# Optimization experiments

Measured on AMD Instinct MI355X. Metric: run time of the kernel, lower is better.

## Reference

```python
import jax, jax.numpy as jnp
import numpy as np

EPS = 1e-5

def layernorm(x):
    mu = jnp.mean(x, axis=-1, keepdims=True)
    var = jnp.var(x, axis=-1, keepdims=True)
    return (x - mu) * jax.lax.rsqrt(var + EPS)

def jagged_to_padded(values, offsets, n):
    # values: [T, D]; offsets: [B+1]; -> [B, n, D] zero-padded
    lengths = offsets[1:] - offsets[:-1]            # [B]
    pos = jnp.arange(n)                             # [n]
    idx = offsets[:-1, None] + pos[None, :]         # [B, n]
    mask = pos[None, :] < lengths[:, None]          # [B, n]
    idx = jnp.clip(idx, 0, values.shape[0] - 1)
    return values[idx] * mask[..., None].astype(values.dtype)

def dense_to_jagged(padded, offsets, total):
    t = jnp.arange(total)
    b = jnp.searchsorted(offsets, t, side='right') - 1   # row of each token
    p = t - offsets[b]                                   # position within row
    return padded[b, p]

def causal_conv(x, w, b):
    # x: [B, n, D]; w: [D, D, 3]; residual + bias + leaky_relu
    xt = jnp.transpose(x, (0, 2, 1))                     # [B, D, n]
    xt = jnp.pad(xt, ((0, 0), (0, 0), (2, 0)))           # causal left pad (k-1)
    y = jax.lax.conv_general_dilated(xt, w, (1,), 'VALID',
                                     dimension_numbers=('NCH', 'OIH', 'NCH'))
    y = y + b[None, :, None]
    y = jnp.transpose(y, (0, 2, 1)) + x                  # residual
    return jax.nn.leaky_relu(y, 0.01)

def setup_inputs() -> dict:
    key = jax.random.key(0)
    ks = jax.random.split(key, 8)
    B, n, D = 32, 4096, 256
    P, H, dA = 512, 8, 64
    T = B * (n // 2)  # equal lengths of 2048
    offsets = (jnp.arange(B + 1, dtype=jnp.int64 if jax.config.read('jax_enable_x64') else jnp.int32) * (n // 2)).astype(jnp.int32)
    return {
        'normed_x': jax.random.normal(ks[0], (T, D), dtype=jnp.float32),
        'conv_w': 0.02 * jax.random.normal(ks[1], (D, D, 3), dtype=jnp.float32),
        'conv_b': 0.02 * jax.random.normal(ks[2], (D,), dtype=jnp.float32),
        'pattern': 0.02 * jax.random.normal(ks[3], (P, D), dtype=jnp.float32),
        'wq': 0.02 * jax.random.normal(ks[4], (H * dA, D), dtype=jnp.float32),
        'wkv': 0.02 * jax.random.normal(ks[5], (2 * H * dA, D), dtype=jnp.float32),
        'wout': jax.random.uniform(ks[6], (D, H * dA), dtype=jnp.float32,
                                   minval=-1.0, maxval=1.0) * np.sqrt(6.0 / (D + H * dA)),
        'bout': jnp.zeros((D,), dtype=jnp.float32),
        'x_offsets': offsets,
        'n': n,
    }

def reference(normed_x, conv_w, conv_b, pattern, wq, wkv, wout, bout, x_offsets, n):
    H, dA = 8, 64
    scale = dA ** (-0.5)
    T = normed_x.shape[0]
    # jagged -> padded, causal conv (residual + leaky_relu), padded -> jagged
    padded = jagged_to_padded(normed_x, x_offsets, n)        # [B, n, D]
    padded = causal_conv(padded, conv_w, conv_b)
    x = dense_to_jagged(padded, x_offsets, T)                # [T, D]
    # pattern layernormed twice (SPRM.forward then xattn.forward)
    pat = layernorm(layernorm(pattern))                      # [P, D]
    x = layernorm(x)
    q = (x @ wq.T).reshape(T, H, dA)                         # [T, H, dA]
    kv = (pat @ wkv.T).reshape(pat.shape[0], H, 2 * dA)
    k, v = kv[..., :dA], kv[..., dA:]                        # [P, H, dA]
    scores = scale * jnp.einsum('nhd,whd->nhw', q, k)        # [T, H, P]
    attn = jax.nn.softmax(scores, axis=-1)
    out = jnp.einsum('nhw,whd->nhd', attn, v).reshape(T, H * dA)
    out = out @ wout.T + bout                                # [T, D]
    return layernorm(out)
```

## Files before the change

kernel.cpp:

```cpp
#include <hip/hip_runtime.h>
#include <hip/hip_bf16.h>
#include <math.h>


#define EPSF 1e-5f

typedef short  s16x8 __attribute__((ext_vector_type(8)));
typedef short  s16x4 __attribute__((ext_vector_type(4)));
typedef float  f32x4 __attribute__((ext_vector_type(4)));

typedef __attribute__((address_space(3))) unsigned int       lds_u32_t;
typedef __attribute__((address_space(1))) const unsigned int glb_u32_t;

__device__ __forceinline__ void gload_lds16(const void* g, void* l) {
    __builtin_amdgcn_global_load_lds((glb_u32_t*)g, (lds_u32_t*)l, 16, 0, 0);
}

__device__ __forceinline__ unsigned short f2bf(float f) {
    union { float f; unsigned u; } v; v.f = f;
    unsigned r = (v.u + 0x7fffu + ((v.u >> 16) & 1u)) >> 16;
    return (unsigned short)r;
}
__device__ __forceinline__ float bf2f(unsigned short h) {
    union { unsigned u; float f; } v; v.u = ((unsigned)h) << 16;
    return v.f;
}
__device__ __forceinline__ unsigned fbits(float f) {
    union { float f; unsigned u; } v; v.f = f; return v.u;
}
__device__ __forceinline__ unsigned pk_hi(float lo, float hi) {
    return __builtin_amdgcn_perm(fbits(hi), fbits(lo), 0x07060302u);
}
__device__ __forceinline__ int inv32(int t) {
    return (t & ~31) | ((t & 0x0C) << 1) | ((t & 0x10) >> 2) | (t & 3);
}

union Bfrag { unsigned u[4]; s16x8 s; };

__global__ void cvt_kernel(const float* __restrict__ wq,
                           const float* __restrict__ wout,
                           const float* __restrict__ cw,
                           short* __restrict__ wq_bf,
                           short* __restrict__ wout_bf,
                           short* __restrict__ wck) {
    const int b = blockIdx.x, tid = threadIdx.x;
    if (b < 256) {
        const int i = ((b & 127) * 256 + tid) * 4;
        const float* src = (b < 128) ? wq : wout;
        short* dst = (b < 128) ? wq_bf : wout_bf;
        const float4 x = *(const float4*)(src + i);
        s16x4 o; o[0] = f2bf(x.x); o[1] = f2bf(x.y); o[2] = f2bf(x.z); o[3] = f2bf(x.w);
        *(s16x4*)(dst + i) = o;
    } else {
        const int idx = (b - 256) * 256 + tid;
        const float* p = cw + (size_t)idx * 3;
        wck[idx]              = (short)f2bf(p[0]);
        wck[65536 + idx]      = (short)f2bf(p[1]);
        wck[131072 + idx]     = (short)f2bf(p[2]);
    }
}

__global__ void pat_kv_kernel(const float* __restrict__ pattern,
                              const float* __restrict__ wkv,
                              short* __restrict__ k_bf,
                              short* __restrict__ v_t) {
    __shared__ __align__(16) float spat[256];
    __shared__ float scr[4];
    const int w = blockIdx.x;
    const int tid = threadIdx.x;
    const int lane = tid & 63, wav = tid >> 6;

    float v = pattern[(size_t)w * 256 + tid];

    float s = v;
    #pragma unroll
    for (int off = 32; off; off >>= 1) s += __shfl_xor(s, off);
    if (lane == 0) scr[wav] = s;
    __syncthreads();
    float mu = (scr[0] + scr[1] + scr[2] + scr[3]) * (1.f / 256.f);
    __syncthreads();
    float d = v - mu;
    float s2 = d * d;
    #pragma unroll
    for (int off = 32; off; off >>= 1) s2 += __shfl_xor(s2, off);
    if (lane == 0) scr[wav] = s2;
    __syncthreads();
    float var = (scr[0] + scr[1] + scr[2] + scr[3]) * (1.f / 256.f);
    float x1 = d * rsqrtf(var + EPSF);
    __syncthreads();

    s = x1;
    #pragma unroll
    for (int off = 32; off; off >>= 1) s += __shfl_xor(s, off);
    if (lane == 0) scr[wav] = s;
    __syncthreads();
    mu = (scr[0] + scr[1] + scr[2] + scr[3]) * (1.f / 256.f);
    __syncthreads();
    d = x1 - mu;
    s2 = d * d;
    #pragma unroll
    for (int off = 32; off; off >>= 1) s2 += __shfl_xor(s2, off);
    if (lane == 0) scr[wav] = s2;
    __syncthreads();
    var = (scr[0] + scr[1] + scr[2] + scr[3]) * (1.f / 256.f);
    float x2 = d * rsqrtf(var + EPSF);

    spat[tid] = x2;
    __syncthreads();

    #pragma unroll
    for (int u = 0; u < 4; u++) {
        const int j = tid + 256 * u;
        const float* wr = wkv + (size_t)j * 256;
        float acc = 0.f;
        for (int i4 = 0; i4 < 64; i4++) {
            float4 w4 = *(const float4*)(wr + i4 * 4);
            float4 x4 = *(const float4*)(&spat[i4 * 4]);
            acc += w4.x * x4.x + w4.y * x4.y + w4.z * x4.z + w4.w * x4.w;
        }
        const int h = j >> 7, r = j & 127;
        if (r < 64) {
            const int c = inv32(r);
            const int ck = w >> 7, crow = w & 127;
            const int un = c >> 3, ph = un ^ (crow & 7);
            k_bf[(size_t)h * 32768 + ck * 8192 + crow * 64 + ph * 8 + (c & 7)]
                = (short)f2bf(acc * 0.125f);
        } else {
            const int rd = r - 64;
            const int c = inv32(w);
            const int ck = c >> 7, cc = c & 127;
            const int un = cc >> 3, ph = un ^ (rd & 15);
            v_t[(size_t)h * 32768 + ck * 8192 + rd * 128 + ph * 8 + (cc & 7)]
                = (short)f2bf(acc);
        }
    }
}

__global__ __launch_bounds__(256, 4)
void conv_ln_kernel(const float* __restrict__ x,
                    const short* __restrict__ wck,
                    const float* __restrict__ cb,
                    short* __restrict__ xn_bf) {
    __shared__ __align__(16) short xs[66 * 268];
    const int tid = threadIdx.x;
    const int r0 = blockIdx.x * 64;
    const int pos0 = r0 & 2047;

    #pragma unroll
    for (int it = 0; it < 17; it++) {
        const int idx = tid + it * 256;
        if (idx < 4224) {
            const int row = idx >> 6, c4 = idx & 63;
            float4 v = {0.f, 0.f, 0.f, 0.f};
            if (pos0 - 2 + row >= 0)
                v = *(const float4*)(x + (size_t)(r0 - 2 + row) * 256 + c4 * 4);
            s16x4 o; o[0] = f2bf(v.x); o[1] = f2bf(v.y); o[2] = f2bf(v.z); o[3] = f2bf(v.w);
            *(s16x4*)(xs + row * 268 + c4 * 4) = o;
        }
    }
    __syncthreads();

    const int lane = tid & 63, w = tid >> 6, g = lane >> 4, cl = lane & 15;

    f32x4 acc[4][4];
    #pragma unroll
    for (int mt = 0; mt < 4; mt++)
        #pragma unroll
        for (int nt = 0; nt < 4; nt++) acc[mt][nt] = (f32x4){0.f, 0.f, 0.f, 0.f};

    #pragma unroll
    for (int kk = 0; kk < 3; kk++) {
        const short* wb = wck + kk * 65536;
        for (int s = 0; s < 8; s++) {
            s16x8 a[4];
            #pragma unroll
            for (int mt = 0; mt < 4; mt++)
                a[mt] = *(const s16x8*)(xs + (mt * 16 + cl + kk) * 268 + s * 32 + g * 8);
            #pragma unroll
            for (int nt = 0; nt < 4; nt++) {
                const s16x8 b = *(const s16x8*)(wb + (size_t)(w * 64 + nt * 16 + cl) * 256 + s * 32 + g * 8);
                #pragma unroll
                for (int mt = 0; mt < 4; mt++)
                    acc[mt][nt] = __builtin_amdgcn_mfma_f32_16x16x32_bf16(a[mt], b, acc[mt][nt], 0, 0, 0);
            }
        }
    }

    #pragma unroll
    for (int nt = 0; nt < 4; nt++) {
        const int col = w * 64 + nt * 16 + cl;
        const float b = cb[col];
        #pragma unroll
        for (int mt = 0; mt < 4; mt++)
            #pragma unroll
            for (int r = 0; r < 4; r++) {
                const int row = mt * 16 + g * 4 + r;
                float y = acc[mt][nt][r] + b + x[(size_t)(r0 + row) * 256 + col];
                acc[mt][nt][r] = (y >= 0.f) ? y : 0.01f * y;
            }
    }
    __syncthreads();
    #pragma unroll
    for (int mt = 0; mt < 4; mt++)
        #pragma unroll
        for (int nt = 0; nt < 4; nt++)
            #pragma unroll
            for (int r = 0; r < 4; r++)
                xs[(mt * 16 + g * 4 + r) * 268 + w * 64 + nt * 16 + cl] =
                    (short)f2bf(acc[mt][nt][r]);
    __syncthreads();

    for (int q = 0; q < 16; q++) {
        const int m = w * 16 + q;
        const s16x4 v4 = *(const s16x4*)(xs + m * 268 + lane * 4);
        const float f0 = bf2f((unsigned short)v4[0]), f1 = bf2f((unsigned short)v4[1]);
        const float f2 = bf2f((unsigned short)v4[2]), f3 = bf2f((unsigned short)v4[3]);
        float s = f0 + f1 + f2 + f3;
        #pragma unroll
        for (int off = 32; off; off >>= 1) s += __shfl_xor(s, off);
        const float mu = s * (1.f / 256.f);
        const float d0 = f0 - mu, d1 = f1 - mu, d2 = f2 - mu, d3 = f3 - mu;
        float vv = d0 * d0 + d1 * d1 + d2 * d2 + d3 * d3;
        #pragma unroll
        for (int off = 32; off; off >>= 1) vv += __shfl_xor(vv, off);
        const float rs = rsqrtf(vv * (1.f / 256.f) + EPSF);
        s16x4 o; o[0] = f2bf(d0 * rs); o[1] = f2bf(d1 * rs);
        o[2] = f2bf(d2 * rs); o[3] = f2bf(d3 * rs);
        *(s16x4*)(xn_bf + (size_t)(r0 + m) * 256 + lane * 4) = o;
    }
}

__global__ __launch_bounds__(256, 2)
void qattn_kernel(const short* __restrict__ xn_bf,
                  const short* __restrict__ wq_bf,
                  const short* __restrict__ k_bf,
                  const short* __restrict__ v_t,
                  short* __restrict__ ao_bf) {
    __shared__ __align__(16) char smem[65536];

    const int tid = threadIdx.x;
    const int lane = tid & 63, w = tid >> 6, g = lane >> 4, cl = lane & 15;
    const int r0 = blockIdx.x * 128;
    const int q0 = r0 + w * 32 + cl;

    const char* kv_base = (w < 2) ? (const char*)k_bf : (const char*)v_t;
    const int   half    = (w & 1) * 8192;

    {
        const char* src = kv_base + half + lane * 16;
        char* dst = smem + w * 8192;
        #pragma unroll
        for (int i = 0; i < 8; i++)
            gload_lds16(src + i * 1024, dst + i * 1024);
    }

    for (int h = 0; h < 8; ++h) {
        f32x4 qacc[2][4];
        #pragma unroll
        for (int u = 0; u < 2; u++)
            #pragma unroll
            for (int nt = 0; nt < 4; nt++) qacc[u][nt] = (f32x4){0.f, 0.f, 0.f, 0.f};
        for (int s = 0; s < 8; ++s) {
            const s16x8 bx0 = *(const s16x8*)(xn_bf + (size_t)q0 * 256 + s * 32 + g * 8);
            const s16x8 bx1 = *(const s16x8*)(xn_bf + ((size_t)q0 + 16) * 256 + s * 32 + g * 8);
            #pragma unroll
            for (int nt = 0; nt < 4; ++nt) {
                const s16x8 aw = *(const s16x8*)(wq_bf + (size_t)(h * 64 + nt * 16 + cl) * 256 + s * 32 + g * 8);
                qacc[0][nt] = __builtin_amdgcn_mfma_f32_16x16x32_bf16(aw, bx0, qacc[0][nt], 0, 0, 0);
                qacc[1][nt] = __builtin_amdgcn_mfma_f32_16x16x32_bf16(aw, bx1, qacc[1][nt], 0, 0, 0);
            }
        }
        Bfrag qB[2][2];
        #pragma unroll
        for (int u = 0; u < 2; ++u)
            #pragma unroll
            for (int s = 0; s < 2; ++s) {
                qB[u][s].u[0] = pk_hi(qacc[u][2 * s][0],     qacc[u][2 * s][1]);
                qB[u][s].u[1] = pk_hi(qacc[u][2 * s][2],     qacc[u][2 * s][3]);
                qB[u][s].u[2] = pk_hi(qacc[u][2 * s + 1][0], qacc[u][2 * s + 1][1]);
                qB[u][s].u[3] = pk_hi(qacc[u][2 * s + 1][2], qacc[u][2 * s + 1][3]);
            }

        float lsum[2] = {0.f, 0.f};
        f32x4 oacc[2][4];
        #pragma unroll
        for (int u = 0; u < 2; u++)
            #pragma unroll
            for (int nd = 0; nd < 4; nd++) oacc[u][nd] = (f32x4){0.f, 0.f, 0.f, 0.f};

        for (int ck = 0; ck < 4; ++ck) {
            const int step = h * 4 + ck;
            const int buf = step & 1;
            __syncthreads();
            if (step + 1 < 32) {
                const int ns = step + 1;
                const char* src = kv_base + (size_t)(ns >> 2) * 65536
                                + (ns & 3) * 16384 + half + lane * 16;
                char* dst = smem + (buf ^ 1) * 32768 + w * 8192;
                #pragma unroll
                for (int i = 0; i < 8; i++)
                    gload_lds16(src + i * 1024, dst + i * 1024);
            }
            const char* kc = smem + buf * 32768;
            const char* vc = kc + 16384;

            f32x4 sa[2][8];
            #pragma unroll
            for (int u = 0; u < 2; u++)
                #pragma unroll
                for (int nt = 0; nt < 8; nt++) sa[u][nt] = (f32x4){0.f, 0.f, 0.f, 0.f};
            #pragma unroll
            for (int nt = 0; nt < 8; nt++) {
                const char* kb = kc + ((nt * 16 + cl) << 7);
                const s16x8 a0 = *(const s16x8*)(kb + ((g       ^ (cl & 7)) << 4));
                const s16x8 a1 = *(const s16x8*)(kb + (((4 + g) ^ (cl & 7)) << 4));
                sa[0][nt] = __builtin_amdgcn_mfma_f32_16x16x32_bf16(a0, qB[0][0].s, sa[0][nt], 0, 0, 0);
                sa[0][nt] = __builtin_amdgcn_mfma_f32_16x16x32_bf16(a1, qB[0][1].s, sa[0][nt], 0, 0, 0);
                sa[1][nt] = __builtin_amdgcn_mfma_f32_16x16x32_bf16(a0, qB[1][0].s, sa[1][nt], 0, 0, 0);
                sa[1][nt] = __builtin_amdgcn_mfma_f32_16x16x32_bf16(a1, qB[1][1].s, sa[1][nt], 0, 0, 0);
            }

            #pragma unroll
            for (int u = 0; u < 2; u++)
                #pragma unroll
                for (int nt = 0; nt < 8; nt++)
                    #pragma unroll
                    for (int r = 0; r < 4; r++) {
                        const float p = __expf(sa[u][nt][r]);
                        lsum[u] += p;
                        sa[u][nt][r] = p;
                    }

            #pragma unroll
            for (int ks = 0; ks < 4; ++ks) {
                Bfrag pB[2];
                #pragma unroll
                for (int u = 0; u < 2; u++) {
                    pB[u].u[0] = pk_hi(sa[u][2 * ks][0],     sa[u][2 * ks][1]);
                    pB[u].u[1] = pk_hi(sa[u][2 * ks][2],     sa[u][2 * ks][3]);
                    pB[u].u[2] = pk_hi(sa[u][2 * ks + 1][0], sa[u][2 * ks + 1][1]);
                    pB[u].u[3] = pk_hi(sa[u][2 * ks + 1][2], sa[u][2 * ks + 1][3]);
                }
                #pragma unroll
                for (int nd = 0; nd < 4; ++nd) {
                    const char* vb = vc + ((nd * 16 + cl) << 8) + (((ks * 4 + g) ^ cl) << 4);
                    const s16x8 av = *(const s16x8*)vb;
                    oacc[0][nd] = __builtin_amdgcn_mfma_f32_16x16x32_bf16(av, pB[0].s, oacc[0][nd], 0, 0, 0);
                    oacc[1][nd] = __builtin_amdgcn_mfma_f32_16x16x32_bf16(av, pB[1].s, oacc[1][nd], 0, 0, 0);
                }
            }
        }

        #pragma unroll
        for (int u = 0; u < 2; ++u) {
            float s = lsum[u];
            s += __shfl_xor(s, 16);
            s += __shfl_xor(s, 32);
            const float inv = 1.f / s;
            const size_t qr = (size_t)(q0 + u * 16);
            #pragma unroll
            for (int nd = 0; nd < 4; ++nd) {
                const float o0 = oacc[u][nd][0] * inv, o1 = oacc[u][nd][1] * inv;
                const float o2 = oacc[u][nd][2] * inv, o3 = oacc[u][nd][3] * inv;
                const unsigned lo = (unsigned)f2bf(o0) | ((unsigned)f2bf(o1) << 16);
                const unsigned hi = (unsigned)f2bf(o2) | ((unsigned)f2bf(o3) << 16);
                short* dst = ao_bf + qr * 512 + h * 64 + nd * 16 + 4 * g;
                *(unsigned*)(dst)     = lo;
                *(unsigned*)(dst + 2) = hi;
            }
        }
    }
}

__global__ __launch_bounds__(256, 4)
void outproj_ln_kernel(const short* __restrict__ ao,
                       const short* __restrict__ wout_bf,
                       const float* __restrict__ bout,
                       float* __restrict__ out) {
    __shared__ __align__(16) char smem[33280];
    short* as = (short*)smem;
    float* ys = (float*)smem;
    const int tid = threadIdx.x;
    const int r0 = blockIdx.x * 32;

    #pragma unroll
    for (int it = 0; it < 8; it++) {
        const int idx = tid + it * 256;
        const int row = idx >> 6, c8 = idx & 63;
        const s16x8 v = *(const s16x8*)(ao + (size_t)(r0 + row) * 512 + c8 * 8);
        *(s16x8*)(as + row * 520 + c8 * 8) = v;
    }
    __syncthreads();

    const int lane = tid & 63, w = tid >> 6, g = lane >> 4, cl = lane & 15;

    f32x4 acc[2][4];
    #pragma unroll
    for (int mt = 0; mt < 2; mt++)
        #pragma unroll
        for (int nt = 0; nt < 4; nt++) acc[mt][nt] = (f32x4){0.f, 0.f, 0.f, 0.f};

    for (int s = 0; s < 16; s++) {
        const s16x8 a0 = *(const s16x8*)(as + cl * 520 + s * 32 + g * 8);
        const s16x8 a1 = *(const s16x8*)(as + (16 + cl) * 520 + s * 32 + g * 8);
        #pragma unroll
        for (int nt = 0; nt < 4; nt++) {
            const s16x8 b = *(const s16x8*)(wout_bf + (size_t)(w * 64 + nt * 16 + cl) * 512 + s * 32 + g * 8);
            acc[0][nt] = __builtin_amdgcn_mfma_f32_16x16x32_bf16(a0, b, acc[0][nt], 0, 0, 0);
            acc[1][nt] = __builtin_amdgcn_mfma_f32_16x16x32_bf16(a1, b, acc[1][nt], 0, 0, 0);
        }
    }
    __syncthreads();

    #pragma unroll
    for (int nt = 0; nt < 4; nt++) {
        const int col = w * 64 + nt * 16 + cl;
        const float b = bout[col];
        #pragma unroll
        for (int mt = 0; mt < 2; mt++)
            #pragma unroll
            for (int r = 0; r < 4; r++)
                ys[(mt * 16 + g * 4 + r) * 260 + col] = acc[mt][nt][r] + b;
    }
    __syncthreads();

    for (int q = 0; q < 8; q++) {
        const int m = w * 8 + q;
        const float4 v4 = *(const float4*)(ys + m * 260 + lane * 4);
        float s = v4.x + v4.y + v4.z + v4.w;
        #pragma unroll
        for (int off = 32; off; off >>= 1) s += __shfl_xor(s, off);
        const float mu = s * (1.f / 256.f);
        const float d0 = v4.x - mu, d1 = v4.y - mu, d2 = v4.z - mu, d3 = v4.w - mu;
        float vv = d0 * d0 + d1 * d1 + d2 * d2 + d3 * d3;
        #pragma unroll
        for (int off = 32; off; off >>= 1) vv += __shfl_xor(vv, off);
        const float rs = rsqrtf(vv * (1.f / 256.f) + EPSF);
        float4 o; o.x = d0 * rs; o.y = d1 * rs; o.z = d2 * rs; o.w = d3 * rs;
        *(float4*)(out + (size_t)(r0 + m) * 256 + lane * 4) = o;
    }
}

extern "C" void kernel_launch(void* const* d_in, const int* in_sizes, int n_in,
                              void* d_out, int out_size, void* d_ws, size_t ws_size,
                              hipStream_t stream) {
    const float* normed_x = (const float*)d_in[0];
    const float* conv_w   = (const float*)d_in[1];
    const float* conv_b   = (const float*)d_in[2];
    const float* pattern  = (const float*)d_in[3];
    const float* wq       = (const float*)d_in[4];
    const float* wkv      = (const float*)d_in[5];
    const float* wout     = (const float*)d_in[6];
    const float* bout     = (const float*)d_in[7];
    const int T = in_sizes[0] / 256;

    char* wsb = (char*)d_ws;
    short* xn_bf  = (short*)(wsb);
    short* ao_bf  = (short*)(wsb + (size_t)33554432);
    short* k_bf   = (short*)(wsb + (size_t)100663296);
    short* v_t    = (short*)(wsb + (size_t)101187584);
    short* wq_bf  = (short*)(wsb + (size_t)101711872);
    short* wout_bf= (short*)(wsb + (size_t)101974016);
    short* wck    = (short*)(wsb + (size_t)102236160);
    float* out    = (float*)d_out;

    cvt_kernel<<<512, 256, 0, stream>>>(wq, wout, conv_w, wq_bf, wout_bf, wck);
    pat_kv_kernel<<<512, 256, 0, stream>>>(pattern, wkv, k_bf, v_t);
    conv_ln_kernel<<<T / 64, 256, 0, stream>>>(normed_x, wck, conv_b, xn_bf);
    qattn_kernel<<<T / 128, 256, 0, stream>>>(xn_bf, wq_bf, k_bf, v_t, ao_bf);
    outproj_ln_kernel<<<T / 32, 256, 0, stream>>>(ao_bf, wout_bf, bout, out);
}
```

Before: 563.0 us.

## Read K/V directly from global memory in attention, drop LDS staging

The attention kernel no longer stages K and V chunks through double-buffered shared memory with async global-to-LDS loads and per-step barriers. Each wave now reads its MFMA operands straight from global memory (relying on L2/L1 since K/V are small and shared by all blocks). K/V are stored unswizzled to match. Blocks shrink to 128 threads (64 queries) with a higher occupancy target, and the score/exp/PV computation is fused per 32-key slice to cut register pressure. The risk is higher global load latency and redundant traffic per wave in place of cheap LDS reads.

```diff
diff --git a/kernel.cpp b/kernel.cpp
--- a/kernel.cpp
+++ b/kernel.cpp
@@ -8,13 +8,6 @@
 typedef short  s16x8 __attribute__((ext_vector_type(8)));
 typedef short  s16x4 __attribute__((ext_vector_type(4)));
 typedef float  f32x4 __attribute__((ext_vector_type(4)));
-
-typedef __attribute__((address_space(3))) unsigned int       lds_u32_t;
-typedef __attribute__((address_space(1))) const unsigned int glb_u32_t;
-
-__device__ __forceinline__ void gload_lds16(const void* g, void* l) {
-    __builtin_amdgcn_global_load_lds((glb_u32_t*)g, (lds_u32_t*)l, 16, 0, 0);
-}
 
 __device__ __forceinline__ unsigned short f2bf(float f) {
     union { float f; unsigned u; } v; v.f = f;
@@ -121,16 +114,11 @@
         const int h = j >> 7, r = j & 127;
         if (r < 64) {
             const int c = inv32(r);
-            const int ck = w >> 7, crow = w & 127;
-            const int un = c >> 3, ph = un ^ (crow & 7);
-            k_bf[(size_t)h * 32768 + ck * 8192 + crow * 64 + ph * 8 + (c & 7)]
-                = (short)f2bf(acc * 0.125f);
+            k_bf[(size_t)h * 32768 + (size_t)w * 64 + c] = (short)f2bf(acc * 0.125f);
         } else {
             const int rd = r - 64;
             const int c = inv32(w);
-            const int ck = c >> 7, cc = c & 127;
-            const int un = cc >> 3, ph = un ^ (rd & 15);
-            v_t[(size_t)h * 32768 + ck * 8192 + rd * 128 + ph * 8 + (cc & 7)]
+            v_t[(size_t)h * 32768 + (size_t)(c >> 7) * 8192 + rd * 128 + (c & 127)]
                 = (short)f2bf(acc);
         }
     }
@@ -230,29 +218,15 @@
     }
 }
 
-__global__ __launch_bounds__(256, 2)
+__global__ __launch_bounds__(128, 3)
 void qattn_kernel(const short* __restrict__ xn_bf,
                   const short* __restrict__ wq_bf,
                   const short* __restrict__ k_bf,
                   const short* __restrict__ v_t,
                   short* __restrict__ ao_bf) {
-    __shared__ __align__(16) char smem[65536];
-
     const int tid = threadIdx.x;
     const int lane = tid & 63, w = tid >> 6, g = lane >> 4, cl = lane & 15;
-    const int r0 = blockIdx.x * 128;
-    const int q0 = r0 + w * 32 + cl;
-
-    const char* kv_base = (w < 2) ? (const char*)k_bf : (const char*)v_t;
-    const int   half    = (w & 1) * 8192;
-
-    {
-        const char* src = kv_base + half + lane * 16;
-        char* dst = smem + w * 8192;
-        #pragma unroll
-        for (int i = 0; i < 8; i++)
-            gload_lds16(src + i * 1024, dst + i * 1024);
-    }
+    const int q0 = blockIdx.x * 64 + w * 32 + cl;
 
     for (int h = 0; h < 8; ++h) {
         f32x4 qacc[2][4];
@@ -288,63 +262,47 @@
             #pragma unroll
             for (int nd = 0; nd < 4; nd++) oacc[u][nd] = (f32x4){0.f, 0.f, 0.f, 0.f};
 
+        const short* kp = k_bf + (size_t)h * 32768;
+        const short* vp = v_t  + (size_t)h * 32768;
+
         for (int ck = 0; ck < 4; ++ck) {
-            const int step = h * 4 + ck;
-            const int buf = step & 1;
-            __syncthreads();
-            if (step + 1 < 32) {
-                const int ns = step + 1;
-                const char* src = kv_base + (size_t)(ns >> 2) * 65536
-                                + (ns & 3) * 16384 + half + lane * 16;
-                char* dst = smem + (buf ^ 1) * 32768 + w * 8192;
+            const short* kc = kp + ck * 8192;
+            const short* vc = vp + ck * 8192;
+
+            #pragma unroll
+            for (int ks = 0; ks < 4; ++ks) {
+                const s16x8 a00 = *(const s16x8*)(kc + ((2 * ks)     * 16 + cl) * 64 + g * 8);
+                const s16x8 a01 = *(const s16x8*)(kc + ((2 * ks)     * 16 + cl) * 64 + 32 + g * 8);
+                const s16x8 a10 = *(const s16x8*)(kc + ((2 * ks + 1) * 16 + cl) * 64 + g * 8);
+                const s16x8 a11 = *(const s16x8*)(kc + ((2 * ks + 1) * 16 + cl) * 64 + 32 + g * 8);
+
+                f32x4 s00 = (f32x4){0.f, 0.f, 0.f, 0.f}, s01 = s00, s10 = s00, s11 = s00;
+                s00 = __builtin_amdgcn_mfma_f32_16x16x32_bf16(a00, qB[0][0].s, s00, 0, 0, 0);
+                s00 = __builtin_amdgcn_mfma_f32_16x16x32_bf16(a01, qB[0][1].s, s00, 0, 0, 0);
+                s01 = __builtin_amdgcn_mfma_f32_16x16x32_bf16(a10, qB[0][0].s, s01, 0, 0, 0);
+                s01 = __builtin_amdgcn_mfma_f32_16x16x32_bf16(a11, qB[0][1].s, s01, 0, 0, 0);
+                s10 = __builtin_amdgcn_mfma_f32_16x16x32_bf16(a00, qB[1][0].s, s10, 0, 0, 0);
+                s10 = __builtin_amdgcn_mfma_f32_16x16x32_bf16(a01, qB[1][1].s, s10, 0, 0, 0);
+                s11 = __builtin_amdgcn_mfma_f32_16x16x32_bf16(a10, qB[1][0].s, s11, 0, 0, 0);
+                s11 = __builtin_amdgcn_mfma_f32_16x16x32_bf16(a11, qB[1][1].s, s11, 0, 0, 0);
+
                 #pragma unroll
-                for (int i = 0; i < 8; i++)
-                    gload_lds16(src + i * 1024, dst + i * 1024);
-            }
-            const char* kc = smem + buf * 32768;
-            const char* vc = kc + 16384;
-
-            f32x4 sa[2][8];
-            #pragma unroll
-            for (int u = 0; u < 2; u++)
-                #pragma unroll
-                for (int nt = 0; nt < 8; nt++) sa[u][nt] = (f32x4){0.f, 0.f, 0.f, 0.f};
-            #pragma unroll
-            for (int nt = 0; nt < 8; nt++) {
-                const char* kb = kc + ((nt * 16 + cl) << 7);
-                const s16x8 a0 = *(const s16x8*)(kb + ((g       ^ (cl & 7)) << 4));
-                const s16x8 a1 = *(const s16x8*)(kb + (((4 + g) ^ (cl & 7)) << 4));
-                sa[0][nt] = __builtin_amdgcn_mfma_f32_16x16x32_bf16(a0, qB[0][0].s, sa[0][nt], 0, 0, 0);
-                sa[0][nt] = __builtin_amdgcn_mfma_f32_16x16x32_bf16(a1, qB[0][1].s, sa[0][nt], 0, 0, 0);
-                sa[1][nt] = __builtin_amdgcn_mfma_f32_16x16x32_bf16(a0, qB[1][0].s, sa[1][nt], 0, 0, 0);
-                sa[1][nt] = __builtin_amdgcn_mfma_f32_16x16x32_bf16(a1, qB[1][1].s, sa[1][nt], 0, 0, 0);
-            }
-
-            #pragma unroll
-            for (int u = 0; u < 2; u++)
-                #pragma unroll
-                for (int nt = 0; nt < 8; nt++)
-                    #pragma unroll
-                    for (int r = 0; r < 4; r++) {
-                        const float p = __expf(sa[u][nt][r]);
-                        lsum[u] += p;
-                        sa[u][nt][r] = p;
-                    }
-
-            #pragma unroll
-            for (int ks = 0; ks < 4; ++ks) {
+                for (int r = 0; r < 4; r++) {
+                    s00[r] = __expf(s00[r]); lsum[0] += s00[r];
+                    s01[r] = __expf(s01[r]); lsum[0] += s01[r];
+                    s10[r] = __expf(s10[r]); lsum[1] += s10[r];
+                    s11[r] = __expf(s11[r]); lsum[1] += s11[r];
+                }
+
                 Bfrag pB[2];
-                #pragma unroll
-                for (int u = 0; u < 2; u++) {
-                    pB[u].u[0] = pk_hi(sa[u][2 * ks][0],     sa[u][2 * ks][1]);
-                    pB[u].u[1] = pk_hi(sa[u][2 * ks][2],     sa[u][2 * ks][3]);
-                    pB[u].u[2] = pk_hi(sa[u][2 * ks + 1][0], sa[u][2 * ks + 1][1]);
-                    pB[u].u[3] = pk_hi(sa[u][2 * ks + 1][2], sa[u][2 * ks + 1][3]);
-                }
+                pB[0].u[0] = pk_hi(s00[0], s00[1]); pB[0].u[1] = pk_hi(s00[2], s00[3]);
+                pB[0].u[2] = pk_hi(s01[0], s01[1]); pB[0].u[3] = pk_hi(s01[2], s01[3]);
+                pB[1].u[0] = pk_hi(s10[0], s10[1]); pB[1].u[1] = pk_hi(s10[2], s10[3]);
+                pB[1].u[2] = pk_hi(s11[0], s11[1]); pB[1].u[3] = pk_hi(s11[2], s11[3]);
+
                 #pragma unroll
                 for (int nd = 0; nd < 4; ++nd) {
-                    const char* vb = vc + ((nd * 16 + cl) << 8) + (((ks * 4 + g) ^ cl) << 4);
-                    const s16x8 av = *(const s16x8*)vb;
+                    const s16x8 av = *(const s16x8*)(vc + (nd * 16 + cl) * 128 + (ks * 4 + g) * 8);
                     oacc[0][nd] = __builtin_amdgcn_mfma_f32_16x16x32_bf16(av, pB[0].s, oacc[0][nd], 0, 0, 0);
                     oacc[1][nd] = __builtin_amdgcn_mfma_f32_16x16x32_bf16(av, pB[1].s, oacc[1][nd], 0, 0, 0);
                 }
@@ -467,6 +425,6 @@
     cvt_kernel<<<512, 256, 0, stream>>>(wq, wout, conv_w, wq_bf, wout_bf, wck);
     pat_kv_kernel<<<512, 256, 0, stream>>>(pattern, wkv, k_bf, v_t);
     conv_ln_kernel<<<T / 64, 256, 0, stream>>>(normed_x, wck, conv_b, xn_bf);
-    qattn_kernel<<<T / 128, 256, 0, stream>>>(xn_bf, wq_bf, k_bf, v_t, ao_bf);
+    qattn_kernel<<<T / 64, 128, 0, stream>>>(xn_bf, wq_bf, k_bf, v_t, ao_bf);
     outproj_ln_kernel<<<T / 32, 256, 0, stream>>>(ao_bf, wout_bf, bout, out);
 }
```

Measured after the change: 657.0 us. +16.7%, slower.
